# Kernel optimization log

Measured on AMD Instinct MI355X. Metric: run time of the kernel, lower is better.

The kernel has to match this reference:

```python
import jax, jax.numpy as jnp
import numpy as np

H = 16      # num_heads
HD = 64     # head_dim
W = 1024    # local window size
G = 256     # number of global tokens
EPS = 1e-6
NEG = -1e30


def setup_inputs() -> dict:
    key = jax.random.key(0)
    ks = jax.random.split(key, 7)
    B, S, D = 1, 8192, 1024
    inner = H * HD
    s = 0.02
    return {
        "x": jax.random.normal(ks[0], (B, S, D), jnp.float32),
        "norm_w": jnp.ones((D,), jnp.float32),
        "w_q": jax.random.normal(ks[1], (D, inner), jnp.float32) * s,
        "w_k": jax.random.normal(ks[2], (D, inner), jnp.float32) * s,
        "w_v": jax.random.normal(ks[3], (D, inner), jnp.float32) * s,
        "w_out": jax.random.normal(ks[4], (inner, D), jnp.float32) * s,
        "scorer_w": jax.random.normal(ks[5], (D, 1), jnp.float32) * s,
        "scorer_b": jnp.zeros((1,), jnp.float32),
    }


def reference(x, norm_w, w_q, w_k, w_v, w_out, scorer_w, scorer_b):
    B, S, D = x.shape
    # pre-norm (RMSNorm)
    h = x * jax.lax.rsqrt(jnp.mean(x * x, axis=-1, keepdims=True) + EPS) * norm_w

    def proj(w):  # [B,S,D] -> [B,H,S,HD]
        return jnp.einsum('bsd,de->bse', h, w).reshape(B, S, H, HD).transpose(0, 2, 1, 3)

    q, k, v = proj(w_q), proj(w_k), proj(w_v)
    scale = HD ** -0.5

    # --- local block attention (non-overlapping causal windows) ---
    nW = S // W
    qw = q.reshape(B, H, nW, W, HD)
    kw = k.reshape(B, H, nW, W, HD)
    vw = v.reshape(B, H, nW, W, HD)
    ll = jnp.einsum('bhnqd,bhnkd->bhnqk', qw, kw) * scale  # [B,H,nW,W,W]
    cm = jnp.tril(jnp.ones((W, W), bool))
    ll = jnp.where(cm, ll, NEG).reshape(B, H, S, W)

    # --- sparse global attention over top-G important tokens ---
    scores = (jnp.einsum('bsd,do->bso', h, scorer_w) + scorer_b)[..., 0]  # [B,S]
    _, idx = jax.lax.top_k(scores, G)                                     # [B,G]
    kg = jnp.take_along_axis(k, idx[:, None, :, None], axis=2)            # [B,H,G,HD]
    vg = jnp.take_along_axis(v, idx[:, None, :, None], axis=2)
    lg = jnp.einsum('bhsd,bhgd->bhsg', q, kg) * scale                     # [B,H,S,G]
    pos = jnp.arange(S)
    gmask = idx[:, None, None, :] <= pos[None, None, :, None]             # causal: global pos <= query pos
    lg = jnp.where(gmask, lg, NEG)

    # --- joint softmax over local window + global tokens ---
    attn = jax.nn.softmax(jnp.concatenate([ll, lg], axis=-1), axis=-1)    # [B,H,S,W+G]
    a_loc = attn[..., :W].reshape(B, H, nW, W, W)
    o = jnp.einsum('bhnqk,bhnkd->bhnqd', a_loc, vw).reshape(B, H, S, HD)
    o = o + jnp.einsum('bhsg,bhgd->bhsd', attn[..., W:], vg)

    o = o.transpose(0, 2, 1, 3).reshape(B, S, H * HD)
    return x + jnp.einsum('bse,ed->bsd', o, w_out)  # residual
```

## Files before the change

### kernel.cpp

```cpp
#include <hip/hip_runtime.h>
#include <stdint.h>

#define S_LEN 8192
#define DIM   1024
#define NH    16
#define HD    64
#define WIN   1024
#define GTOK  256
#define QKV_STRIDE (3 * DIM)

typedef __attribute__((ext_vector_type(8))) short bf16x8;
typedef __attribute__((ext_vector_type(4))) float f32x4;
typedef __attribute__((ext_vector_type(16))) float f32x16;
typedef unsigned short u16;

__device__ __forceinline__ u16 f2bf(float f) {
  union { float f; uint32_t u; } v; v.f = f;
  uint32_t r = v.u + 0x7fffu + ((v.u >> 16) & 1u);
  return (u16)(r >> 16);
}
__device__ __forceinline__ float bf2f(u16 b) {
  union { uint32_t u; float f; } v; v.u = ((uint32_t)b) << 16;
  return v.f;
}
__device__ __forceinline__ uint32_t cvtpk(float a, float b) {
  uint32_t r;
  asm("v_cvt_pk_bf16_f32 %0, %1, %2" : "=v"(r) : "v"(a), "v"(b));
  return r;
}

__device__ __forceinline__ void gload_lds16(const void* g, void* l) {
  __builtin_amdgcn_global_load_lds((const __attribute__((address_space(1))) void*)g,
                                   (__attribute__((address_space(3))) void*)l, 16, 0, 0);
}

__global__ __launch_bounds__(256) void rmsnorm_score_kernel(
    const float* __restrict__ x, const float* __restrict__ nw,
    const float* __restrict__ sw, const float* __restrict__ sb,
    u16* __restrict__ h, float* __restrict__ scores) {
  int row = blockIdx.x, tid = threadIdx.x;
  const float4* xr = (const float4*)(x + (size_t)row * DIM);
  float4 v = xr[tid];
  float ss = v.x * v.x + v.y * v.y + v.z * v.z + v.w * v.w;
#pragma unroll
  for (int o = 32; o >= 1; o >>= 1) ss += __shfl_xor(ss, o);
  __shared__ float red[4], red2[4];
  int wv = tid >> 6;
  if ((tid & 63) == 0) red[wv] = ss;
  __syncthreads();
  ss = red[0] + red[1] + red[2] + red[3];
  float rn = rsqrtf(ss * (1.0f / DIM) + 1e-6f);
  float4 w4 = ((const float4*)nw)[tid];
  float h0 = v.x * rn * w4.x, h1 = v.y * rn * w4.y;
  float h2 = v.z * rn * w4.z, h3 = v.w * rn * w4.w;
  uint64_t pack = (uint64_t)f2bf(h0) | ((uint64_t)f2bf(h1) << 16) |
                  ((uint64_t)f2bf(h2) << 32) | ((uint64_t)f2bf(h3) << 48);
  *(uint64_t*)(h + (size_t)row * DIM + tid * 4) = pack;
  float4 s4 = ((const float4*)sw)[tid];
  float sc = h0 * s4.x + h1 * s4.y + h2 * s4.z + h3 * s4.w;
#pragma unroll
  for (int o = 32; o >= 1; o >>= 1) sc += __shfl_xor(sc, o);
  if ((tid & 63) == 0) red2[wv] = sc;
  __syncthreads();
  if (tid == 0) scores[row] = red2[0] + red2[1] + red2[2] + red2[3] + sb[0];
}

__global__ __launch_bounds__(256) void transpose_w_kernel(
    const float* __restrict__ wq, const float* __restrict__ wk,
    const float* __restrict__ wv, const float* __restrict__ wo,
    u16* __restrict__ wqkvT, u16* __restrict__ woutT) {
  __shared__ float tile[32][33];
  int z = blockIdx.z;
  const float* src = (z == 0) ? wq : (z == 1) ? wk : (z == 2) ? wv : wo;
  u16* dst = (z < 3) ? (wqkvT + (size_t)z * DIM * DIM) : woutT;
  int tx = threadIdx.x, ty = threadIdx.y;
  int n0 = blockIdx.x * 32, k0 = blockIdx.y * 32;
#pragma unroll
  for (int i = 0; i < 4; i++)
    tile[ty + i * 8][tx] = src[(size_t)(k0 + ty + i * 8) * DIM + n0 + tx];
  __syncthreads();
#pragma unroll
  for (int i = 0; i < 4; i++)
    dst[(size_t)(n0 + ty + i * 8) * DIM + k0 + tx] = f2bf(tile[tx][ty + i * 8]);
}

__global__ __launch_bounds__(256) void topk_init_kernel(int* __restrict__ cnt) {
  cnt[blockIdx.x * 256 + threadIdx.x] = 0;
}

__global__ __launch_bounds__(256) void topk_count_kernel(
    const float* __restrict__ scores, int* __restrict__ cnt) {
  __shared__ float sj[1024];
  int jbase = blockIdx.y * 1024;
  for (int t = threadIdx.x; t < 1024; t += 256) sj[t] = scores[jbase + t];
  __syncthreads();
  int i = blockIdx.x * 256 + threadIdx.x;
  float my = scores[i];
  int c = 0;
  const float4* s4 = (const float4*)sj;
#pragma unroll 4
  for (int j = 0; j < 256; j++) {
    float4 v = s4[j];
    int b = jbase + j * 4;
    c += (v.x > my) || (v.x == my && (b + 0) < i);
    c += (v.y > my) || (v.y == my && (b + 1) < i);
    c += (v.z > my) || (v.z == my && (b + 2) < i);
    c += (v.w > my) || (v.w == my && (b + 3) < i);
  }
  if (c) atomicAdd(&cnt[i], c);
}

__global__ __launch_bounds__(256) void topk_scatter_kernel(
    const int* __restrict__ cnt, int* __restrict__ gidx) {
  int i = blockIdx.x * 256 + threadIdx.x;
  int c = cnt[i];
  if (c < GTOK) gidx[c] = i;
}

__global__ __launch_bounds__(128) void gather_kernel(
    const u16* __restrict__ qkv, const int* __restrict__ gidx,
    u16* __restrict__ kg, u16* __restrict__ vg) {
  int g = blockIdx.x, t = threadIdx.x;
  size_t src = (size_t)gidx[g] * QKV_STRIDE;
  *(bf16x8*)(kg + (size_t)g * DIM + t * 8) = *(const bf16x8*)(qkv + src + DIM + t * 8);
  *(bf16x8*)(vg + (size_t)g * DIM + t * 8) = *(const bf16x8*)(qkv + src + 2 * DIM + t * 8);
}

template <int RESID>
__global__ __launch_bounds__(512, 2) void gemm256_kernel(
    const u16* __restrict__ A, const u16* __restrict__ B,
    u16* __restrict__ Cb, float* __restrict__ Cf, const float* __restrict__ X,
    int M, int N, int K) {
  __shared__ u16 As[2][256 * 64];
  __shared__ u16 Bs[2][256 * 64];
  const int tid = threadIdx.x;
  const int wave = tid >> 6, lane = tid & 63;
  const int l15 = lane & 15, l4 = lane >> 4;
  const int wr = wave >> 2, wc = wave & 3;
  const int mbase = blockIdx.x * 256, nbase = blockIdx.y * 256;

  const int srow = (lane >> 3);
  const int schunk = lane & 7;
  const int gchunk8 = (schunk ^ srow) * 8;

  f32x4 acc[8][4] = {};

  const int nt = K >> 6;
#pragma unroll
  for (int l = 0; l < 4; l++) {
    int rbase = (wave * 4 + l) * 8;
    int row = rbase + srow;
    gload_lds16(A + (size_t)(mbase + row) * K + gchunk8,
                &As[0][(size_t)(wave * 4 + l) * 512]);
    gload_lds16(B + (size_t)(nbase + row) * K + gchunk8,
                &Bs[0][(size_t)(wave * 4 + l) * 512]);
  }
  asm volatile("s_waitcnt vmcnt(0)" ::: "memory");
  __syncthreads();

  for (int t = 0; t < nt; t++) {
    const int p = t & 1;
    if (t + 1 < nt) {
      const int kt = (t + 1) << 6;
#pragma unroll
      for (int l = 0; l < 4; l++) {
        int rbase = (wave * 4 + l) * 8;
        int row = rbase + srow;
        gload_lds16(A + (size_t)(mbase + row) * K + kt + gchunk8,
                    &As[p ^ 1][(size_t)(wave * 4 + l) * 512]);
        gload_lds16(B + (size_t)(nbase + row) * K + kt + gchunk8,
                    &Bs[p ^ 1][(size_t)(wave * 4 + l) * 512]);
      }
    }
    const u16* Ab = &As[p][0];
    const u16* Bb = &Bs[p][0];
    bf16x8 bfr[4][2];
#pragma unroll
    for (int nf = 0; nf < 4; nf++) {
      int row = wc * 64 + nf * 16 + l15;
#pragma unroll
      for (int kk = 0; kk < 2; kk++)
        bfr[nf][kk] = *(const bf16x8*)(Bb + row * 64 + (((kk * 4 + l4) ^ (l15 & 7)) * 8));
    }
#pragma unroll
    for (int mh = 0; mh < 2; mh++) {
      bf16x8 af[4][2];
#pragma unroll
      for (int mi = 0; mi < 4; mi++) {
        int row = wr * 128 + (mh * 4 + mi) * 16 + l15;
#pragma unroll
        for (int kk = 0; kk < 2; kk++)
          af[mi][kk] = *(const bf16x8*)(Ab + row * 64 + (((kk * 4 + l4) ^ (l15 & 7)) * 8));
      }
      __builtin_amdgcn_s_setprio(1);
#pragma unroll
      for (int mi = 0; mi < 4; mi++)
#pragma unroll
        for (int nf = 0; nf < 4; nf++)
#pragma unroll
          for (int kk = 0; kk < 2; kk++)
            acc[mh * 4 + mi][nf] =
                __builtin_amdgcn_mfma_f32_16x16x32_bf16(af[mi][kk], bfr[nf][kk],
                                                        acc[mh * 4 + mi][nf], 0, 0, 0);
      __builtin_amdgcn_s_setprio(0);
    }
    asm volatile("s_waitcnt vmcnt(0)" ::: "memory");
    __syncthreads();
  }

#pragma unroll
  for (int mf = 0; mf < 8; mf++) {
#pragma unroll
    for (int nf = 0; nf < 4; nf++) {
#pragma unroll
      for (int r = 0; r < 4; r++) {
        int row = mbase + wr * 128 + mf * 16 + l4 * 4 + r;
        int col = nbase + wc * 64 + nf * 16 + l15;
        float v = acc[mf][nf][r];
        if (RESID) Cf[(size_t)row * N + col] = X[(size_t)row * N + col] + v;
        else       Cb[(size_t)row * N + col] = f2bf(v);
      }
    }
  }
}

__global__ __launch_bounds__(512) void attn_kernel(
    const u16* __restrict__ qkv, const u16* __restrict__ kg,
    const u16* __restrict__ vg, const int* __restrict__ gidx,
    u16* __restrict__ o) {
  __shared__ u16 kT[2][64][72];
  __shared__ u16 vT[2][64][72];
  __shared__ int gposLds[2][64];
  const int tid = threadIdx.x, wave = tid >> 6, lane = tid & 63;
  const int l31 = lane & 31, hi = lane >> 5;
  const int win = blockIdx.x >> 1, pair = blockIdx.x & 1;
  const int wbase = win * WIN;
  const int hoff = blockIdx.y * HD;

  const int skey = tid >> 3, sd8 = (tid & 7) * 8;
  const int vcol = skey ^ ((sd8 >> 4) << 4);

  bf16x8 nk, nv;
  int ng = 0;
  {
    const u16* base = qkv + (size_t)(wbase + skey) * QKV_STRIDE + hoff + sd8;
    nk = *(const bf16x8*)(base + DIM);
    nv = *(const bf16x8*)(base + 2 * DIM);
  }

  for (int sp = 0; sp < 2; sp++) {
    const int j = sp ? (3 - pair) : pair;
    const int qsbase = wbase + j * 256;
    const int nLocal = (j + 1) * 4;
    const int nTiles = nLocal + GTOK / 64;
    const int qrow = qsbase + wave * 32 + l31;
    const int qwmax = qsbase + wave * 32 + 31;

    bf16x8 qf[4];
    {
      const float SC2 = 0.125f * 1.44269504088896f;
      const u16* qptr = qkv + (size_t)qrow * QKV_STRIDE + hoff + hi * 8;
#pragma unroll
      for (int ks = 0; ks < 4; ks++) {
        bf16x8 raw = *(const bf16x8*)(qptr + ks * 16);
        bf16x8 sc;
#pragma unroll
        for (int jj = 0; jj < 8; jj++) sc[jj] = (short)f2bf(bf2f((u16)raw[jj]) * SC2);
        qf[ks] = sc;
      }
    }

    f32x16 acc0 = {}, acc1 = {};
    float mr = -3.0e38f, lr = 0.f;

    __syncthreads();

    for (int t = 0; t < nTiles; t++) {
      const int p = t & 1;
      const bool isLocal = (t < nLocal);
      const int tbase = wbase + t * 64;
      *(bf16x8*)(&kT[p][skey][sd8]) = nk;
#pragma unroll
      for (int jj = 0; jj < 8; jj++) vT[p][sd8 + jj][vcol] = (u16)nv[jj];
      if (!isLocal && tid < 64) gposLds[p][tid] = ng;
      {
        const int nt = t + 1;
        const u16 *ksrc = nullptr, *vsrc = nullptr;
        if (nt < nLocal) {
          const u16* base = qkv + (size_t)(wbase + nt * 64 + skey) * QKV_STRIDE + hoff + sd8;
          ksrc = base + DIM; vsrc = base + 2 * DIM;
        } else if (nt < nTiles) {
          size_t grow = (size_t)((nt - nLocal) * 64 + skey) * DIM + hoff + sd8;
          ksrc = kg + grow; vsrc = vg + grow;
          if (tid < 64) ng = gidx[(nt - nLocal) * 64 + tid];
        } else if (sp == 0) {
          const u16* base = qkv + (size_t)(wbase + skey) * QKV_STRIDE + hoff + sd8;
          ksrc = base + DIM; vsrc = base + 2 * DIM;
        }
        if (ksrc) { nk = *(const bf16x8*)(ksrc); nv = *(const bf16x8*)(vsrc); }
      }
      __syncthreads();

      if (isLocal && tbase > qwmax) continue;

      float sv[32];
      __builtin_amdgcn_s_setprio(1);
#pragma unroll
      for (int kb = 0; kb < 2; kb++) {
        const u16* krow = &kT[p][kb * 32 + l31][hi * 8];
        bf16x8 k0 = *(const bf16x8*)(krow);
        bf16x8 k1 = *(const bf16x8*)(krow + 16);
        bf16x8 k2 = *(const bf16x8*)(krow + 32);
        bf16x8 k3 = *(const bf16x8*)(krow + 48);
        f32x16 z = {};
        z = __builtin_amdgcn_mfma_f32_32x32x16_bf16(k0, qf[0], z, 0, 0, 0);
        z = __builtin_amdgcn_mfma_f32_32x32x16_bf16(k1, qf[1], z, 0, 0, 0);
        z = __builtin_amdgcn_mfma_f32_32x32x16_bf16(k2, qf[2], z, 0, 0, 0);
        z = __builtin_amdgcn_mfma_f32_32x32x16_bf16(k3, qf[3], z, 0, 0, 0);
#pragma unroll
        for (int r = 0; r < 16; r++) sv[kb * 16 + r] = z[r];
      }
      __builtin_amdgcn_s_setprio(0);

      if (isLocal) {
        const int lim = qrow - tbase;
        if (lim < 63) {
#pragma unroll
          for (int kb = 0; kb < 2; kb++)
#pragma unroll
            for (int r = 0; r < 16; r++) {
              int crow = kb * 32 + (r & 3) + 8 * (r >> 2) + 4 * hi;
              if (crow > lim) sv[kb * 16 + r] = -3.0e38f;
            }
        }
      } else {
#pragma unroll
        for (int kb = 0; kb < 2; kb++)
#pragma unroll
          for (int r = 0; r < 16; r++) {
            int kpos = gposLds[p][kb * 32 + (r & 3) + 8 * (r >> 2) + 4 * hi];
            if (kpos > qrow) sv[kb * 16 + r] = -3.0e38f;
          }
      }

      float m0 = sv[0], m1 = sv[1], m2 = sv[2], m3 = sv[3];
#pragma unroll
      for (int i = 4; i < 32; i += 4) {
        m0 = fmaxf(m0, sv[i]);     m1 = fmaxf(m1, sv[i + 1]);
        m2 = fmaxf(m2, sv[i + 2]); m3 = fmaxf(m3, sv[i + 3]);
      }
      float vmax = fmaxf(fmaxf(m0, m1), fmaxf(m2, m3));
      vmax = fmaxf(vmax, __shfl_xor(vmax, 32));
      if (__any(vmax > mr + 11.0f)) {
        float mn = fmaxf(mr, vmax);
        float al = exp2f(mr - mn);
        lr *= al;
        mr = mn;
#pragma unroll
        for (int i = 0; i < 16; i++) { acc0[i] *= al; acc1[i] *= al; }
      }
      float s0 = 0.f, s1 = 0.f, s2 = 0.f, s3 = 0.f;
#pragma unroll
      for (int i = 0; i < 32; i += 4) {
        float p0 = exp2f(sv[i] - mr),     p1 = exp2f(sv[i + 1] - mr);
        float p2 = exp2f(sv[i + 2] - mr), p3 = exp2f(sv[i + 3] - mr);
        sv[i] = p0; sv[i + 1] = p1; sv[i + 2] = p2; sv[i + 3] = p3;
        s0 += p0; s1 += p1; s2 += p2; s3 += p3;
      }
      float ps = (s0 + s1) + (s2 + s3);
      ps += __shfl_xor(ps, 32);
      lr += ps;

      bf16x8 pf[4];
#pragma unroll
      for (int q4 = 0; q4 < 4; q4++) {
        int b = q4 * 8;
        uint32_t w0 = cvtpk(sv[b + 0], sv[b + 1]);
        uint32_t w1 = cvtpk(sv[b + 2], sv[b + 3]);
        uint32_t w2 = cvtpk(sv[b + 4], sv[b + 5]);
        uint32_t w3 = cvtpk(sv[b + 6], sv[b + 7]);
        uint32_t w0s = __shfl_xor((int)w0, 32), w2s = __shfl_xor((int)w2, 32);
        uint32_t w1s = __shfl_xor((int)w1, 32), w3s = __shfl_xor((int)w3, 32);
        union { uint32_t w[4]; bf16x8 v; } u;
        u.w[0] = hi ? w2s : w0;
        u.w[1] = hi ? w3s : w1;
        u.w[2] = hi ? w2 : w0s;
        u.w[3] = hi ? w3 : w1s;
        pf[q4] = u.v;
      }

      __builtin_amdgcn_s_setprio(1);
#pragma unroll
      for (int dblk = 0; dblk < 2; dblk++) {
        const int swz = (dblk * 2 + (l31 >> 4)) << 4;
        const u16* vrow = &vT[p][dblk * 32 + l31][0];
        f32x16 a = dblk ? acc1 : acc0;
#pragma unroll
        for (int ksg = 0; ksg < 4; ksg++) {
          bf16x8 vf = *(const bf16x8*)(vrow + ((ksg * 16 + hi * 8) ^ swz));
          a = __builtin_amdgcn_mfma_f32_32x32x16_bf16(vf, pf[ksg], a, 0, 0, 0);
        }
        if (dblk) acc1 = a; else acc0 = a;
      }
      __builtin_amdgcn_s_setprio(0);
    }

    float inv = 1.0f / lr;
#pragma unroll
    for (int dblk = 0; dblk < 2; dblk++) {
      f32x16 a = dblk ? acc1 : acc0;
#pragma unroll
      for (int g = 0; g < 4; g++) {
        uint64_t pk = (uint64_t)f2bf(a[g * 4 + 0] * inv)
                    | ((uint64_t)f2bf(a[g * 4 + 1] * inv) << 16)
                    | ((uint64_t)f2bf(a[g * 4 + 2] * inv) << 32)
                    | ((uint64_t)f2bf(a[g * 4 + 3] * inv) << 48);
        *(uint64_t*)(o + (size_t)qrow * DIM + hoff + dblk * 32 + g * 8 + 4 * hi) = pk;
      }
    }
  }
}

extern "C" void kernel_launch(void* const* d_in, const int* in_sizes, int n_in,
                              void* d_out, int out_size, void* d_ws, size_t ws_size,
                              hipStream_t stream) {
  const float* x  = (const float*)d_in[0];
  const float* nw = (const float*)d_in[1];
  const float* wq = (const float*)d_in[2];
  const float* wk = (const float*)d_in[3];
  const float* wv = (const float*)d_in[4];
  const float* wo = (const float*)d_in[5];
  const float* sw = (const float*)d_in[6];
  const float* sb = (const float*)d_in[7];
  float* out = (float*)d_out;

  char* ws = (char*)d_ws;
  size_t off = 0;
  auto alloc = [&](size_t b) {
    char* p = ws + off;
    off = (off + b + 255) & ~(size_t)255;
    return p;
  };
  u16*   h      = (u16*)alloc((size_t)S_LEN * DIM * 2);
  u16*   wqkvT  = (u16*)alloc((size_t)3 * DIM * DIM * 2);
  u16*   woutT  = (u16*)alloc((size_t)DIM * DIM * 2);
  u16*   qkv    = (u16*)alloc((size_t)S_LEN * 3 * DIM * 2);
  u16*   obuf   = (u16*)alloc((size_t)S_LEN * DIM * 2);
  float* scores = (float*)alloc((size_t)S_LEN * 4);
  int*   gidx   = (int*)alloc((size_t)GTOK * 4);
  int*   cnt    = (int*)alloc((size_t)S_LEN * 4);
  u16*   kgbuf  = (u16*)alloc((size_t)GTOK * DIM * 2);
  u16*   vgbuf  = (u16*)alloc((size_t)GTOK * DIM * 2);

  transpose_w_kernel<<<dim3(32, 32, 4), dim3(32, 8), 0, stream>>>(wq, wk, wv, wo, wqkvT, woutT);
  rmsnorm_score_kernel<<<dim3(S_LEN), dim3(256), 0, stream>>>(x, nw, sw, sb, h, scores);
  topk_init_kernel<<<dim3(S_LEN / 256), dim3(256), 0, stream>>>(cnt);
  topk_count_kernel<<<dim3(32, 8), dim3(256), 0, stream>>>(scores, cnt);
  topk_scatter_kernel<<<dim3(S_LEN / 256), dim3(256), 0, stream>>>(cnt, gidx);
  gemm256_kernel<0><<<dim3(32, 12), dim3(512), 0, stream>>>(h, wqkvT, qkv, nullptr, nullptr,
                                                            S_LEN, 3 * DIM, DIM);
  gather_kernel<<<dim3(GTOK), dim3(128), 0, stream>>>(qkv, gidx, kgbuf, vgbuf);
  attn_kernel<<<dim3(16, NH), dim3(512), 0, stream>>>(qkv, kgbuf, vgbuf, gidx, obuf);
  gemm256_kernel<1><<<dim3(32, 4), dim3(512), 0, stream>>>(obuf, woutT, nullptr, out, x,
                                                           S_LEN, DIM, DIM);
}
```

Baseline: 230.3 us.

## Retile GEMM to 256x128 with triple-buffered LDS and re-split attention blocks

The GEMM tile shrinks from 256x256 to 256x128, doubling the grid, and the LDS pipeline moves from double to triple buffering with partial vmcnt waits and raw barriers. The attention kernel drops to 256 threads, splits each window into eight 128-row query chunks instead of four 256-row chunks, and doubles its grid. It also reworks the K/V LDS staging with XOR swizzles and packed paired-key V writes to cut bank conflicts and store count. The intent is more blocks across the CUs and deeper load/compute overlap, at the cost of less reuse per tile and more redundant K/V loads per block.

```diff
diff --git a/kernel.cpp b/kernel.cpp
--- a/kernel.cpp
+++ b/kernel.cpp
@@ -13,6 +13,7 @@
 typedef __attribute__((ext_vector_type(4))) float f32x4;
 typedef __attribute__((ext_vector_type(16))) float f32x16;
 typedef unsigned short u16;
+typedef uint32_t u32;
 
 __device__ __forceinline__ u16 f2bf(float f) {
   union { float f; uint32_t u; } v; v.f = f;
@@ -131,50 +132,46 @@
     const u16* __restrict__ A, const u16* __restrict__ B,
     u16* __restrict__ Cb, float* __restrict__ Cf, const float* __restrict__ X,
     int M, int N, int K) {
-  __shared__ u16 As[2][256 * 64];
-  __shared__ u16 Bs[2][256 * 64];
+  __shared__ __align__(16) u16 As[3][256 * 64];
+  __shared__ __align__(16) u16 Bs[3][128 * 64];
   const int tid = threadIdx.x;
   const int wave = tid >> 6, lane = tid & 63;
   const int l15 = lane & 15, l4 = lane >> 4;
-  const int wr = wave >> 2, wc = wave & 3;
-  const int mbase = blockIdx.x * 256, nbase = blockIdx.y * 256;
-
-  const int srow = (lane >> 3);
-  const int schunk = lane & 7;
-  const int gchunk8 = (schunk ^ srow) * 8;
-
-  f32x4 acc[8][4] = {};
+  const int wr = wave >> 1, wc = wave & 1;
+  const int mbase = blockIdx.x * 256, nbase = blockIdx.y * 128;
+  const int srow = lane >> 3, schunk = lane & 7;
+  const int gcol = (schunk ^ srow) * 8;
+
+  auto stage = [&](int tt, int b) {
+    const int kt = tt << 6;
+#pragma unroll
+    for (int l = 0; l < 4; l++) {
+      int row = wave * 32 + l * 8;
+      gload_lds16(A + (size_t)(mbase + row + srow) * K + kt + gcol, &As[b][row * 64]);
+    }
+#pragma unroll
+    for (int l = 0; l < 2; l++) {
+      int row = wave * 16 + l * 8;
+      gload_lds16(B + (size_t)(nbase + row + srow) * K + kt + gcol, &Bs[b][row * 64]);
+    }
+  };
 
   const int nt = K >> 6;
-#pragma unroll
-  for (int l = 0; l < 4; l++) {
-    int rbase = (wave * 4 + l) * 8;
-    int row = rbase + srow;
-    gload_lds16(A + (size_t)(mbase + row) * K + gchunk8,
-                &As[0][(size_t)(wave * 4 + l) * 512]);
-    gload_lds16(B + (size_t)(nbase + row) * K + gchunk8,
-                &Bs[0][(size_t)(wave * 4 + l) * 512]);
-  }
-  asm volatile("s_waitcnt vmcnt(0)" ::: "memory");
-  __syncthreads();
-
+  f32x4 acc[4][4] = {};
+
+  stage(0, 0);
+  stage(1, 1);
+  asm volatile("s_waitcnt vmcnt(6)" ::: "memory");
+  __builtin_amdgcn_s_barrier();
+  __builtin_amdgcn_sched_barrier(0);
+
+  int cur = 0;
   for (int t = 0; t < nt; t++) {
-    const int p = t & 1;
-    if (t + 1 < nt) {
-      const int kt = (t + 1) << 6;
-#pragma unroll
-      for (int l = 0; l < 4; l++) {
-        int rbase = (wave * 4 + l) * 8;
-        int row = rbase + srow;
-        gload_lds16(A + (size_t)(mbase + row) * K + kt + gchunk8,
-                    &As[p ^ 1][(size_t)(wave * 4 + l) * 512]);
-        gload_lds16(B + (size_t)(nbase + row) * K + kt + gchunk8,
-                    &Bs[p ^ 1][(size_t)(wave * 4 + l) * 512]);
-      }
-    }
-    const u16* Ab = &As[p][0];
-    const u16* Bb = &Bs[p][0];
-    bf16x8 bfr[4][2];
+    int pre = cur + 2; if (pre >= 3) pre -= 3;
+    if (t + 2 < nt) stage(t + 2, pre);
+    const u16* Ab = &As[cur][0];
+    const u16* Bb = &Bs[cur][0];
+    bf16x8 bfr[4][2], af[4][2];
 #pragma unroll
     for (int nf = 0; nf < 4; nf++) {
       int row = wc * 64 + nf * 16 + l15;
@@ -183,40 +180,40 @@
         bfr[nf][kk] = *(const bf16x8*)(Bb + row * 64 + (((kk * 4 + l4) ^ (l15 & 7)) * 8));
     }
 #pragma unroll
-    for (int mh = 0; mh < 2; mh++) {
-      bf16x8 af[4][2];
-#pragma unroll
-      for (int mi = 0; mi < 4; mi++) {
-        int row = wr * 128 + (mh * 4 + mi) * 16 + l15;
+    for (int mi = 0; mi < 4; mi++) {
+      int row = wr * 64 + mi * 16 + l15;
+#pragma unroll
+      for (int kk = 0; kk < 2; kk++)
+        af[mi][kk] = *(const bf16x8*)(Ab + row * 64 + (((kk * 4 + l4) ^ (l15 & 7)) * 8));
+    }
+    __builtin_amdgcn_s_setprio(1);
+#pragma unroll
+    for (int mi = 0; mi < 4; mi++)
+#pragma unroll
+      for (int nf = 0; nf < 4; nf++)
 #pragma unroll
         for (int kk = 0; kk < 2; kk++)
-          af[mi][kk] = *(const bf16x8*)(Ab + row * 64 + (((kk * 4 + l4) ^ (l15 & 7)) * 8));
-      }
-      __builtin_amdgcn_s_setprio(1);
-#pragma unroll
-      for (int mi = 0; mi < 4; mi++)
-#pragma unroll
-        for (int nf = 0; nf < 4; nf++)
-#pragma unroll
-          for (int kk = 0; kk < 2; kk++)
-            acc[mh * 4 + mi][nf] =
-                __builtin_amdgcn_mfma_f32_16x16x32_bf16(af[mi][kk], bfr[nf][kk],
-                                                        acc[mh * 4 + mi][nf], 0, 0, 0);
-      __builtin_amdgcn_s_setprio(0);
-    }
-    asm volatile("s_waitcnt vmcnt(0)" ::: "memory");
-    __syncthreads();
+          acc[mi][nf] = __builtin_amdgcn_mfma_f32_16x16x32_bf16(af[mi][kk], bfr[nf][kk],
+                                                                acc[mi][nf], 0, 0, 0);
+    __builtin_amdgcn_s_setprio(0);
+    if (t + 1 < nt) {
+      if (t + 2 < nt) asm volatile("s_waitcnt vmcnt(6)" ::: "memory");
+      else            asm volatile("s_waitcnt vmcnt(0)" ::: "memory");
+      __builtin_amdgcn_s_barrier();
+      __builtin_amdgcn_sched_barrier(0);
+    }
+    cur = (cur + 1 == 3) ? 0 : cur + 1;
   }
 
 #pragma unroll
-  for (int mf = 0; mf < 8; mf++) {
+  for (int mi = 0; mi < 4; mi++) {
 #pragma unroll
     for (int nf = 0; nf < 4; nf++) {
 #pragma unroll
       for (int r = 0; r < 4; r++) {
-        int row = mbase + wr * 128 + mf * 16 + l4 * 4 + r;
+        int row = mbase + wr * 64 + mi * 16 + l4 * 4 + r;
         int col = nbase + wc * 64 + nf * 16 + l15;
-        float v = acc[mf][nf][r];
+        float v = acc[mi][nf][r];
         if (RESID) Cf[(size_t)row * N + col] = X[(size_t)row * N + col] + v;
         else       Cb[(size_t)row * N + col] = f2bf(v);
       }
@@ -224,34 +221,41 @@
   }
 }
 
-__global__ __launch_bounds__(512) void attn_kernel(
+__global__ __launch_bounds__(256) void attn_kernel(
     const u16* __restrict__ qkv, const u16* __restrict__ kg,
     const u16* __restrict__ vg, const int* __restrict__ gidx,
     u16* __restrict__ o) {
-  __shared__ u16 kT[2][64][72];
-  __shared__ u16 vT[2][64][72];
+  __shared__ __align__(16) u16 kT[2][64][72];
+  __shared__ __align__(16) u16 vT[2][64][72];
   __shared__ int gposLds[2][64];
   const int tid = threadIdx.x, wave = tid >> 6, lane = tid & 63;
   const int l31 = lane & 31, hi = lane >> 5;
-  const int win = blockIdx.x >> 1, pair = blockIdx.x & 1;
+  const int win = blockIdx.x >> 2, pr = blockIdx.x & 3;
   const int wbase = win * WIN;
   const int hoff = blockIdx.y * HD;
-
-  const int skey = tid >> 3, sd8 = (tid & 7) * 8;
-  const int vcol = skey ^ ((sd8 >> 4) << 4);
-
-  bf16x8 nk, nv;
+  const int ks = (l31 >> 3) & 3;
+
+  const int skey = tid >> 2;
+  const int kc0 = (tid & 3) * 2;
+  const int kswz = (skey >> 3) & 3;
+  const int kp = tid & 31, dblk = tid >> 5;
+  const int vcol = kp ^ ((dblk & 3) << 2);
+
+  bf16x8 nk0, nk1, nva, nvb;
   int ng = 0;
   {
-    const u16* base = qkv + (size_t)(wbase + skey) * QKV_STRIDE + hoff + sd8;
-    nk = *(const bf16x8*)(base + DIM);
-    nv = *(const bf16x8*)(base + 2 * DIM);
+    const u16* kb = qkv + (size_t)(wbase + skey) * QKV_STRIDE + DIM + hoff;
+    nk0 = *(const bf16x8*)(kb + kc0 * 8);
+    nk1 = *(const bf16x8*)(kb + kc0 * 8 + 8);
+    const u16* vb = qkv + (size_t)(wbase + 2 * kp) * QKV_STRIDE + 2 * DIM + hoff + dblk * 8;
+    nva = *(const bf16x8*)(vb);
+    nvb = *(const bf16x8*)(vb + QKV_STRIDE);
   }
 
   for (int sp = 0; sp < 2; sp++) {
-    const int j = sp ? (3 - pair) : pair;
-    const int qsbase = wbase + j * 256;
-    const int nLocal = (j + 1) * 4;
+    const int j = sp ? (7 - pr) : pr;
+    const int qsbase = wbase + j * 128;
+    const int nLocal = (j + 1) * 2;
     const int nTiles = nLocal + GTOK / 64;
     const int qrow = qsbase + wave * 32 + l31;
     const int qwmax = qsbase + wave * 32 + 31;
@@ -261,12 +265,12 @@
       const float SC2 = 0.125f * 1.44269504088896f;
       const u16* qptr = qkv + (size_t)qrow * QKV_STRIDE + hoff + hi * 8;
 #pragma unroll
-      for (int ks = 0; ks < 4; ks++) {
-        bf16x8 raw = *(const bf16x8*)(qptr + ks * 16);
+      for (int ksub = 0; ksub < 4; ksub++) {
+        bf16x8 raw = *(const bf16x8*)(qptr + ksub * 16);
         bf16x8 sc;
 #pragma unroll
         for (int jj = 0; jj < 8; jj++) sc[jj] = (short)f2bf(bf2f((u16)raw[jj]) * SC2);
-        qf[ks] = sc;
+        qf[ksub] = sc;
       }
     }
 
@@ -279,27 +283,40 @@
       const int p = t & 1;
       const bool isLocal = (t < nLocal);
       const int tbase = wbase + t * 64;
-      *(bf16x8*)(&kT[p][skey][sd8]) = nk;
-#pragma unroll
-      for (int jj = 0; jj < 8; jj++) vT[p][sd8 + jj][vcol] = (u16)nv[jj];
+      *(bf16x8*)(&kT[p][skey][(kc0 ^ kswz) * 8]) = nk0;
+      *(bf16x8*)(&kT[p][skey][((kc0 + 1) ^ kswz) * 8]) = nk1;
+#pragma unroll
+      for (int jj = 0; jj < 8; jj++) {
+        uint32_t pk2 = (u16)nva[jj] | ((uint32_t)(u16)nvb[jj] << 16);
+        ((u32*)&vT[p][dblk * 8 + jj][0])[vcol] = pk2;
+      }
       if (!isLocal && tid < 64) gposLds[p][tid] = ng;
       {
-        const int nt = t + 1;
+        const int ntile = t + 1;
         const u16 *ksrc = nullptr, *vsrc = nullptr;
-        if (nt < nLocal) {
-          const u16* base = qkv + (size_t)(wbase + nt * 64 + skey) * QKV_STRIDE + hoff + sd8;
-          ksrc = base + DIM; vsrc = base + 2 * DIM;
-        } else if (nt < nTiles) {
-          size_t grow = (size_t)((nt - nLocal) * 64 + skey) * DIM + hoff + sd8;
-          ksrc = kg + grow; vsrc = vg + grow;
-          if (tid < 64) ng = gidx[(nt - nLocal) * 64 + tid];
+        size_t vstride = QKV_STRIDE;
+        if (ntile < nLocal) {
+          ksrc = qkv + (size_t)(wbase + ntile * 64 + skey) * QKV_STRIDE + DIM + hoff + kc0 * 8;
+          vsrc = qkv + (size_t)(wbase + ntile * 64 + 2 * kp) * QKV_STRIDE + 2 * DIM + hoff + dblk * 8;
+        } else if (ntile < nTiles) {
+          ksrc = kg + (size_t)((ntile - nLocal) * 64 + skey) * DIM + hoff + kc0 * 8;
+          vsrc = vg + (size_t)((ntile - nLocal) * 64 + 2 * kp) * DIM + hoff + dblk * 8;
+          vstride = DIM;
+          if (tid < 64) ng = gidx[(ntile - nLocal) * 64 + tid];
         } else if (sp == 0) {
-          const u16* base = qkv + (size_t)(wbase + skey) * QKV_STRIDE + hoff + sd8;
-          ksrc = base + DIM; vsrc = base + 2 * DIM;
+          ksrc = qkv + (size_t)(wbase + skey) * QKV_STRIDE + DIM + hoff + kc0 * 8;
+          vsrc = qkv + (size_t)(wbase + 2 * kp) * QKV_STRIDE + 2 * DIM + hoff + dblk * 8;
         }
-        if (ksrc) { nk = *(const bf16x8*)(ksrc); nv = *(const bf16x8*)(vsrc); }
-      }
-      __syncthreads();
+        if (ksrc) {
+          nk0 = *(const bf16x8*)(ksrc);
+          nk1 = *(const bf16x8*)(ksrc + 8);
+          nva = *(const bf16x8*)(vsrc);
+          nvb = *(const bf16x8*)(vsrc + vstride);
+        }
+      }
+      asm volatile("s_waitcnt lgkmcnt(0)" ::: "memory");
+      __builtin_amdgcn_s_barrier();
+      __builtin_amdgcn_sched_barrier(0);
 
       if (isLocal && tbase > qwmax) continue;
 
@@ -307,11 +324,11 @@
       __builtin_amdgcn_s_setprio(1);
 #pragma unroll
       for (int kb = 0; kb < 2; kb++) {
-        const u16* krow = &kT[p][kb * 32 + l31][hi * 8];
-        bf16x8 k0 = *(const bf16x8*)(krow);
-        bf16x8 k1 = *(const bf16x8*)(krow + 16);
-        bf16x8 k2 = *(const bf16x8*)(krow + 32);
-        bf16x8 k3 = *(const bf16x8*)(krow + 48);
+        const u16* krow = &kT[p][kb * 32 + l31][0];
+        bf16x8 k0 = *(const bf16x8*)(krow + ((hi + 0) ^ ks) * 8);
+        bf16x8 k1 = *(const bf16x8*)(krow + ((hi + 2) ^ ks) * 8);
+        bf16x8 k2 = *(const bf16x8*)(krow + ((hi + 4) ^ ks) * 8);
+        bf16x8 k3 = *(const bf16x8*)(krow + ((hi + 6) ^ ks) * 8);
         f32x16 z = {};
         z = __builtin_amdgcn_mfma_f32_32x32x16_bf16(k0, qf[0], z, 0, 0, 0);
         z = __builtin_amdgcn_mfma_f32_32x32x16_bf16(k1, qf[1], z, 0, 0, 0);
@@ -391,31 +408,30 @@
 
       __builtin_amdgcn_s_setprio(1);
 #pragma unroll
-      for (int dblk = 0; dblk < 2; dblk++) {
-        const int swz = (dblk * 2 + (l31 >> 4)) << 4;
-        const u16* vrow = &vT[p][dblk * 32 + l31][0];
-        f32x16 a = dblk ? acc1 : acc0;
+      for (int dsel = 0; dsel < 2; dsel++) {
+        const u16* vrow = &vT[p][dsel * 32 + l31][0];
+        f32x16 a = dsel ? acc1 : acc0;
 #pragma unroll
         for (int ksg = 0; ksg < 4; ksg++) {
-          bf16x8 vf = *(const bf16x8*)(vrow + ((ksg * 16 + hi * 8) ^ swz));
+          bf16x8 vf = *(const bf16x8*)(vrow + (((ksg * 2 + hi) ^ ks) * 8));
           a = __builtin_amdgcn_mfma_f32_32x32x16_bf16(vf, pf[ksg], a, 0, 0, 0);
         }
-        if (dblk) acc1 = a; else acc0 = a;
+        if (dsel) acc1 = a; else acc0 = a;
       }
       __builtin_amdgcn_s_setprio(0);
     }
 
     float inv = 1.0f / lr;
 #pragma unroll
-    for (int dblk = 0; dblk < 2; dblk++) {
-      f32x16 a = dblk ? acc1 : acc0;
+    for (int dsel = 0; dsel < 2; dsel++) {
+      f32x16 a = dsel ? acc1 : acc0;
 #pragma unroll
       for (int g = 0; g < 4; g++) {
         uint64_t pk = (uint64_t)f2bf(a[g * 4 + 0] * inv)
                     | ((uint64_t)f2bf(a[g * 4 + 1] * inv) << 16)
                     | ((uint64_t)f2bf(a[g * 4 + 2] * inv) << 32)
                     | ((uint64_t)f2bf(a[g * 4 + 3] * inv) << 48);
-        *(uint64_t*)(o + (size_t)qrow * DIM + hoff + dblk * 32 + g * 8 + 4 * hi) = pk;
+        *(uint64_t*)(o + (size_t)qrow * DIM + hoff + dsel * 32 + g * 8 + 4 * hi) = pk;
       }
     }
   }
@@ -457,10 +473,10 @@
   topk_init_kernel<<<dim3(S_LEN / 256), dim3(256), 0, stream>>>(cnt);
   topk_count_kernel<<<dim3(32, 8), dim3(256), 0, stream>>>(scores, cnt);
   topk_scatter_kernel<<<dim3(S_LEN / 256), dim3(256), 0, stream>>>(cnt, gidx);
-  gemm256_kernel<0><<<dim3(32, 12), dim3(512), 0, stream>>>(h, wqkvT, qkv, nullptr, nullptr,
+  gemm256_kernel<0><<<dim3(32, 24), dim3(512), 0, stream>>>(h, wqkvT, qkv, nullptr, nullptr,
                                                             S_LEN, 3 * DIM, DIM);
   gather_kernel<<<dim3(GTOK), dim3(128), 0, stream>>>(qkv, gidx, kgbuf, vgbuf);
-  attn_kernel<<<dim3(16, NH), dim3(512), 0, stream>>>(qkv, kgbuf, vgbuf, gidx, obuf);
-  gemm256_kernel<1><<<dim3(32, 4), dim3(512), 0, stream>>>(obuf, woutT, nullptr, out, x,
+  attn_kernel<<<dim3(32, NH), dim3(256), 0, stream>>>(qkv, kgbuf, vgbuf, gidx, obuf);
+  gemm256_kernel<1><<<dim3(32, 8), dim3(512), 0, stream>>>(obuf, woutT, nullptr, out, x,
                                                            S_LEN, DIM, DIM);
 }
```

Result: slower. 255.0 us (+10.8%).
